# Kernel optimization log

Measured on AMD Instinct MI355X. Metric: run time of the kernel, lower is better.

Reference implementation:

```python
import jax, jax.numpy as jnp
import numpy as np
from jax import lax

EPS = 1e-5
DN = ('NCHW', 'OIHW', 'NCHW')


def setup_inputs() -> dict:
    key = jax.random.key(0)
    ks = jax.random.split(key, 26)
    f = lambda k, shape: jax.random.normal(k, shape, dtype=jnp.float32) * 0.05
    u = lambda k, shape: jax.random.uniform(k, shape, jnp.float32, 0.5, 1.5)
    B = 512
    return {
        'x': jax.random.normal(ks[0], (B, 3, 32, 32), jnp.float32),
        'conv1_w': f(ks[1], (64, 3, 3, 3)), 'conv1_b': f(ks[2], (64,)),
        'bn1_g': 1.0 + f(ks[3], (64,)), 'bn1_b': f(ks[4], (64,)),
        'bn1_m': f(ks[5], (64,)), 'bn1_v': u(ks[6], (64,)),
        'conv2_w': f(ks[7], (256, 64, 3, 3)), 'conv2_b': f(ks[8], (256,)),
        'bna_g': 1.0 + f(ks[9], (64, 4)), 'bna_b': f(ks[10], (64, 4)),
        'bna_m': f(ks[11], (64, 4)), 'bna_v': u(ks[12], (64, 4)),
        'tconv_w': f(ks[13], (64, 8, 4, 3, 3)), 'tconv_b': f(ks[14], (64, 8)),
        'bnb_g': 1.0 + f(ks[15], (64, 8)), 'bnb_b': f(ks[16], (64, 8)),
        'bnb_m': f(ks[17], (64, 8)), 'bnb_v': u(ks[18], (64, 8)),
        'lin_w': f(ks[19], (64, 9, 1152)), 'lin_b': f(ks[20], (64, 9)),
        'fc1_w': f(ks[21], (512, 576)), 'fc1_b': f(ks[22], (512,)),
        'fc2_w': f(ks[23], (100, 512)), 'fc2_b': f(ks[24], (100,)),
    }


def reference(x, conv1_w, conv1_b, bn1_g, bn1_b, bn1_m, bn1_v,
              conv2_w, conv2_b,
              bna_g, bna_b, bna_m, bna_v, tconv_w, tconv_b,
              bnb_g, bnb_b, bnb_m, bnb_v, lin_w, lin_b,
              fc1_w, fc1_b, fc2_w, fc2_b):
    B = x.shape[0]
    # features: Conv(3->64,k3) -> ReLU -> BN(64) -> Conv(64->256,k3) -> ReLU -> MaxPool2
    h = lax.conv_general_dilated(x, conv1_w, (1, 1), 'VALID', dimension_numbers=DN)
    h = jax.nn.relu(h + conv1_b[None, :, None, None])  # [B,64,30,30]
    h = (h - bn1_m[None, :, None, None]) * lax.rsqrt(bn1_v + EPS)[None, :, None, None] \
        * bn1_g[None, :, None, None] + bn1_b[None, :, None, None]
    h = lax.conv_general_dilated(h, conv2_w, (1, 1), 'VALID', dimension_numbers=DN)
    h = jax.nn.relu(h + conv2_b[None, :, None, None])  # [B,256,28,28]
    h = lax.reduce_window(h, -jnp.inf, lax.max, (1, 1, 2, 2), (1, 1, 2, 2), 'VALID')  # [B,256,14,14]

    # 64 towers: BN2d(4) -> Conv(4->8,k3) -> BN2d(8) -> Flatten -> Linear(1152->9)
    f4 = h.reshape(B, 64, 4, 14, 14)
    f4 = (f4 - bna_m[None, :, :, None, None]) * lax.rsqrt(bna_v + EPS)[None, :, :, None, None] \
        * bna_g[None, :, :, None, None] + bna_b[None, :, :, None, None]
    # grouped conv fuses all 64 towers: out channels 64*8=512, 4 in-channels per group
    t = lax.conv_general_dilated(f4.reshape(B, 256, 14, 14), tconv_w.reshape(512, 4, 3, 3),
                                 (1, 1), 'VALID', dimension_numbers=DN, feature_group_count=64)
    t = t + tconv_b.reshape(512)[None, :, None, None]  # [B,512,12,12]
    t = t.reshape(B, 64, 8, 12, 12)
    t = (t - bnb_m[None, :, :, None, None]) * lax.rsqrt(bnb_v + EPS)[None, :, :, None, None] \
        * bnb_g[None, :, :, None, None] + bnb_b[None, :, :, None, None]
    flat = t.reshape(B, 64, 8 * 12 * 12)
    tow = jnp.einsum('btf,tof->bto', flat, lin_w) + lin_b[None]  # [B,64,9]
    z = tow.reshape(B, 576)

    # classifier (dropout = identity in eval)
    h1 = jax.nn.relu(z @ fc1_w.T + fc1_b)
    return h1 @ fc2_w.T + fc2_b
```

## Files before the change

kernel.cpp:

```cpp
#include <hip/hip_runtime.h>
#include <hip/hip_bf16.h>

#define EPS 1e-5f

typedef __attribute__((ext_vector_type(8))) short bf16x8;
typedef __attribute__((ext_vector_type(4))) float f32x4;

__device__ __forceinline__ float b2f(unsigned short u) {
  union { unsigned int i; float f; } v; v.i = ((unsigned int)u) << 16; return v.f;
}
__device__ __forceinline__ unsigned short f2bu(float f) {
  __hip_bfloat16 h = __float2bfloat16(f);
  return *reinterpret_cast<unsigned short*>(&h);
}

__device__ __forceinline__ void g2l16(const void* g, void* l) {
  __builtin_amdgcn_global_load_lds(
      (__attribute__((address_space(1))) void*)((unsigned long long)g),
      (__attribute__((address_space(3))) void*)((unsigned long long)l), 16, 0, 0);
}

__global__ __launch_bounds__(256) void k_prep(
    const float* __restrict__ x, const float* __restrict__ w1,
    const float* __restrict__ cb, const float* __restrict__ bg,
    const float* __restrict__ bb, const float* __restrict__ bm,
    const float* __restrict__ bv, __hip_bfloat16* __restrict__ h1,
    const float* __restrict__ w2, __hip_bfloat16* __restrict__ w2s,
    const float* __restrict__ fw1, unsigned int* __restrict__ w1p,
    const float* __restrict__ fw2, unsigned int* __restrict__ w2p,
    const float* __restrict__ lw, const float* __restrict__ lb,
    const float* __restrict__ tw, const float* __restrict__ tb,
    const float* __restrict__ bag, const float* __restrict__ bab,
    const float* __restrict__ bam, const float* __restrict__ bav,
    const float* __restrict__ bbg, const float* __restrict__ bbb,
    const float* __restrict__ bbm, const float* __restrict__ bbv,
    float* __restrict__ Weff, float* __restrict__ beff) {
  __shared__ __align__(16) char smem[43008];
  int tid = threadIdx.x;
  int bi = blockIdx.x;

  if (bi < 64) {
    int t = bi;
    float* lws = (float*)smem;
    float* tws = (float*)(smem + 41472);
    float* part = (float*)(smem + 42624);
    {
      const float4* src = (const float4*)(lw + (size_t)t * 9 * 1152);
      float4* dst = (float4*)lws;
      for (int i = tid; i < 2592; i += 256) dst[i] = src[i];
    }
    for (int i = tid; i < 288; i += 256) {
      int o8 = i / 36, c = (i % 36) / 9, kk = i % 9;
      float sa = bag[t * 4 + c] * rsqrtf(bav[t * 4 + c] + EPS);
      float sb = bbg[t * 8 + o8] * rsqrtf(bbv[t * 8 + o8] + EPS);
      tws[i] = tw[((t * 8 + o8) * 4 + c) * 9 + kk] * sa * sb;
    }
    __syncthreads();
    if (tid < 252) {
      int j = tid / 28;
      int rem = tid % 28;
      int c = rem / 7, q = rem % 7;
      float acc[2][14];
#pragma unroll
      for (int pr = 0; pr < 2; pr++)
#pragma unroll
        for (int ix = 0; ix < 14; ix++) acc[pr][ix] = 0.f;
#pragma unroll 1
      for (int o8 = 0; o8 < 8; o8++) {
        float twr[9];
#pragma unroll
        for (int kk = 0; kk < 9; kk++) twr[kk] = tws[o8 * 36 + c * 9 + kk];
        float lwc[4][16];
#pragma unroll
        for (int cr = 0; cr < 4; cr++) {
          int y = 2 * q - 2 + cr;
          bool vld = (y >= 0) & (y <= 11);
          int ya = vld ? y : 0;
          const float* bp = lws + j * 1152 + o8 * 144 + ya * 12;
          float4 A = *(const float4*)bp;
          float4 B = *(const float4*)(bp + 4);
          float4 C = *(const float4*)(bp + 8);
          lwc[cr][0] = 0.f; lwc[cr][1] = 0.f; lwc[cr][14] = 0.f; lwc[cr][15] = 0.f;
          lwc[cr][2] = vld ? A.x : 0.f;  lwc[cr][3] = vld ? A.y : 0.f;
          lwc[cr][4] = vld ? A.z : 0.f;  lwc[cr][5] = vld ? A.w : 0.f;
          lwc[cr][6] = vld ? B.x : 0.f;  lwc[cr][7] = vld ? B.y : 0.f;
          lwc[cr][8] = vld ? B.z : 0.f;  lwc[cr][9] = vld ? B.w : 0.f;
          lwc[cr][10] = vld ? C.x : 0.f; lwc[cr][11] = vld ? C.y : 0.f;
          lwc[cr][12] = vld ? C.z : 0.f; lwc[cr][13] = vld ? C.w : 0.f;
        }
#pragma unroll
        for (int ky = 0; ky < 3; ky++)
#pragma unroll
          for (int kx = 0; kx < 3; kx++) {
            float wv = twr[ky * 3 + kx];
#pragma unroll
            for (int pr = 0; pr < 2; pr++)
#pragma unroll
              for (int ix = 0; ix < 14; ix++)
                acc[pr][ix] += lwc[pr - ky + 2][ix - kx + 2] * wv;
          }
      }
#pragma unroll
      for (int pr = 0; pr < 2; pr++)
#pragma unroll
        for (int ix = 0; ix < 14; ix++)
          Weff[(((size_t)(t * 9 + j)) * 196 + (2 * q + pr) * 14 + ix) * 4 + c] = acc[pr][ix];
    }
    if (tid < 72) {
      int j = tid / 8, o8 = tid % 8;
      float s = 0.f;
      const float* bp = lws + j * 1152 + o8 * 144;
      for (int i = 0; i < 144; i++) s += bp[i];
      float sb = bbg[t * 8 + o8] * rsqrtf(bbv[t * 8 + o8] + EPS);
      float bfov = sb * tb[t * 8 + o8] + bbb[t * 8 + o8] - bbm[t * 8 + o8] * sb;
      for (int c2 = 0; c2 < 4; c2++) {
        float sa2 = bag[t * 4 + c2] * rsqrtf(bav[t * 4 + c2] + EPS);
        float ha = bab[t * 4 + c2] - bam[t * 4 + c2] * sa2;
        float wsum = 0.f;
        for (int k = 0; k < 9; k++) wsum += tw[((t * 8 + o8) * 4 + c2) * 9 + k];
        bfov += sb * wsum * ha;
      }
      part[tid] = bfov * s;
    }
    __syncthreads();
    if (tid < 9) {
      float acc = lb[t * 9 + tid];
      for (int o8 = 0; o8 < 8; o8++) acc += part[tid * 8 + o8];
      beff[t * 9 + tid] = acc;
    }
  } else if (bi < 576) {
    int b = bi - 64;
    float* xs = (float*)smem;
    float* wsm = (float*)(smem + 13824);
    {
      const float4* src = (const float4*)(x + (size_t)b * 3072);
      for (int i = tid; i < 768; i += 256) {
        int ic = i >> 8, r = (i >> 3) & 31, v = i & 7;
        *(float4*)(xs + (ic * 32 + r) * 36 + v * 4) = src[i];
      }
      const float4* wsrc = (const float4*)w1;
      float4* wdst = (float4*)wsm;
      for (int i = tid; i < 432; i += 256) wdst[i] = wsrc[i];
    }
    __syncthreads();
    int oc = tid & 63;
    int xg = tid >> 6;
    float wr[27];
#pragma unroll
    for (int q = 0; q < 27; q++) wr[q] = wsm[oc * 27 + q];
    float bias = cb[oc];
    float sc = bg[oc] * rsqrtf(bv[oc] + EPS);
    float sh = bb[oc] - bm[oc] * sc;
    float rx[3][3][12];
#pragma unroll
    for (int ic = 0; ic < 3; ic++)
#pragma unroll
      for (int s = 0; s < 2; s++) {
        const float* rp = xs + (ic * 32 + s) * 36 + xg * 8;
        float4 A = *(const float4*)rp, B = *(const float4*)(rp + 4), C = *(const float4*)(rp + 8);
        rx[ic][s][0] = A.x; rx[ic][s][1] = A.y; rx[ic][s][2] = A.z; rx[ic][s][3] = A.w;
        rx[ic][s][4] = B.x; rx[ic][s][5] = B.y; rx[ic][s][6] = B.z; rx[ic][s][7] = B.w;
        rx[ic][s][8] = C.x; rx[ic][s][9] = C.y; rx[ic][s][10] = C.z; rx[ic][s][11] = C.w;
      }
    int nst = (xg == 3) ? 6 : 8;
    __hip_bfloat16* dst0 = h1 + (((size_t)b * 30) * 30 + xg * 8) * 64 + oc;
#pragma unroll 1
    for (int y3 = 0; y3 < 10; y3++) {
#pragma unroll
      for (int s = 0; s < 3; s++) {
        int y = y3 * 3 + s;
        int ls = (s + 2) % 3;
#pragma unroll
        for (int ic = 0; ic < 3; ic++) {
          const float* rp = xs + (ic * 32 + (y + 2)) * 36 + xg * 8;
          float4 A = *(const float4*)rp, B = *(const float4*)(rp + 4), C = *(const float4*)(rp + 8);
          rx[ic][ls][0] = A.x; rx[ic][ls][1] = A.y; rx[ic][ls][2] = A.z; rx[ic][ls][3] = A.w;
          rx[ic][ls][4] = B.x; rx[ic][ls][5] = B.y; rx[ic][ls][6] = B.z; rx[ic][ls][7] = B.w;
          rx[ic][ls][8] = C.x; rx[ic][ls][9] = C.y; rx[ic][ls][10] = C.z; rx[ic][ls][11] = C.w;
        }
        float o[8];
#pragma unroll
        for (int j = 0; j < 8; j++) o[j] = bias;
#pragma unroll
        for (int ic = 0; ic < 3; ic++)
#pragma unroll
          for (int ky = 0; ky < 3; ky++) {
            int sl = (s + ky) % 3;
#pragma unroll
            for (int kx = 0; kx < 3; kx++) {
              float wv = wr[ic * 9 + ky * 3 + kx];
#pragma unroll
              for (int j = 0; j < 8; j++) o[j] += rx[ic][sl][j + kx] * wv;
            }
          }
        __hip_bfloat16* dst = dst0 + (size_t)y * 30 * 64;
#pragma unroll
        for (int j = 0; j < 8; j++)
          if (j < nst) dst[(size_t)j * 64] = __float2bfloat16(fmaxf(o[j], 0.f) * sc + sh);
      }
    }
  } else if (bi < 1152) {
    int g = (bi - 576) * 256 + tid;
    int kk = g >> 14;
    int rem = g & 16383;
    int oc = rem >> 6, e = rem & 63;
    int es = e ^ ((oc & 7) << 3);
    w2s[(kk * 256 + oc) * 64 + es] = __float2bfloat16(w2[(oc * 64 + e) * 9 + kk]);
  } else {
    int g = (bi - 1152) * 256 + tid;
    {
      int kp = g >> 9, o = g & 511;
      unsigned int lo = f2bu(fw1[o * 576 + 2 * kp]);
      unsigned int hi = f2bu(fw1[o * 576 + 2 * kp + 1]);
      w1p[g] = lo | (hi << 16);
    }
    if (g < 25600) {
      int kp = g / 100, o = g % 100;
      unsigned int lo = f2bu(fw2[o * 512 + 2 * kp]);
      unsigned int hi = f2bu(fw2[o * 512 + 2 * kp + 1]);
      w2p[g] = lo | (hi << 16);
    }
  }
}

__global__ __launch_bounds__(512) void k2_conv2(
    const __hip_bfloat16* __restrict__ h1, const __hip_bfloat16* __restrict__ w2s,
    const float* __restrict__ c2b, __hip_bfloat16* __restrict__ pT) {
  __shared__ __align__(16) char lds[81920];
  int tid = threadIdx.x;
  int bi = blockIdx.x;
  int b = bi / 14, yp = bi % 14;
  int l = tid & 63, w = tid >> 6;

  int r = tid >> 3;
  int rc = r < 56 ? r : 55;
  int yl = rc >= 28 ? 1 : 0;
  int xx = rc - yl * 28;
  int ael = ((tid & 7) << 3) ^ ((rc & 7) << 3);
  const __hip_bfloat16* aSrc0 =
      h1 + (((size_t)(b * 30 + yp * 2 + yl)) * 30 + xx) * 64 + ael;
  const char* bSrc0 = (const char*)w2s;

  f32x4 acc[4][2];
#pragma unroll
  for (int m = 0; m < 4; m++)
#pragma unroll
    for (int n = 0; n < 2; n++) acc[m][n] = (f32x4){0.f, 0.f, 0.f, 0.f};

#define STAGE(kk, s)                                                            \
  {                                                                             \
    g2l16(aSrc0 + (((kk) / 3) * 30 + ((kk) % 3)) * 64,                          \
          lds + (s)*8192 + tid * 16);                                           \
    const char* bs = bSrc0 + (kk)*32768;                                        \
    _Pragma("unroll") for (int q = 0; q < 4; q++)                               \
        g2l16(bs + q * 8192 + tid * 16,                                         \
              lds + 16384 + (s)*32768 + q * 8192 + tid * 16);                   \
  }

  STAGE(0, 0);
#pragma unroll
  for (int c = 0; c < 9; c++) {
    __syncthreads();
    if (c < 8) STAGE(c + 1, (c + 1) & 1);
    char* aB = lds + (c & 1) * 8192;
    char* bB = lds + 16384 + (c & 1) * 32768;
#pragma unroll
    for (int ks = 0; ks < 2; ks++) {
      bf16x8 af[4], bfr[2];
      int kb = (ks * 32 + ((l >> 4) * 8)) * 2;
#pragma unroll
      for (int m = 0; m < 4; m++) {
        int row = m * 16 + (l & 15);
        af[m] = *(const bf16x8*)(aB + row * 128 + (kb ^ ((row & 7) << 4)));
      }
#pragma unroll
      for (int n = 0; n < 2; n++) {
        int oc = w * 32 + n * 16 + (l & 15);
        bfr[n] = *(const bf16x8*)(bB + oc * 128 + (kb ^ ((oc & 7) << 4)));
      }
#pragma unroll
      for (int m = 0; m < 4; m++)
#pragma unroll
        for (int n = 0; n < 2; n++)
          acc[m][n] = __builtin_amdgcn_mfma_f32_16x16x32_bf16(af[m], bfr[n], acc[m][n], 0, 0, 0);
    }
  }
#undef STAGE
  __syncthreads();

  float* ep = (float*)(lds) + w * 2112;
#pragma unroll
  for (int n = 0; n < 2; n++) {
    int col = n * 16 + (l & 15);
    float bias = c2b[w * 32 + col];
#pragma unroll
    for (int m = 0; m < 4; m++)
#pragma unroll
      for (int i = 0; i < 4; i++) {
        int row = m * 16 + ((l >> 4) * 4) + i;
        ep[row * 33 + col] = fmaxf(acc[m][n][i] + bias, 0.f);
      }
  }
  __syncthreads();
  unsigned short* pool = (unsigned short*)(lds + 69632);
#pragma unroll
  for (int q = 0; q < 7; q++) {
    int xp = (l >> 5) * 7 + q;
    int col = l & 31;
    int base0 = (2 * xp) * 33 + col;
    float m0 = fmaxf(fmaxf(ep[base0], ep[base0 + 33]),
                     fmaxf(ep[base0 + 28 * 33], ep[base0 + 29 * 33]));
    pool[(w * 32 + col) * 14 + xp] = f2bu(m0);
  }
  __syncthreads();
  if (tid < 448) {
    int t = tid / 7, sub = tid - t * 7;
    union { unsigned short s[8]; uint4 v; } pk;
#pragma unroll
    for (int e = 0; e < 8; e++) {
      int ee = sub * 8 + e;
      pk.s[e] = pool[(t * 4 + (ee & 3)) * 14 + (ee >> 2)];
    }
    *(uint4*)((char*)pT + ((size_t)(t * 512 + b)) * 1568 + yp * 112 + sub * 16) = pk.v;
  }
}

__global__ __launch_bounds__(576) void k3_towers(
    const __hip_bfloat16* __restrict__ pT, const float* __restrict__ Weff,
    const float* __restrict__ beff, float* __restrict__ z) {
  __shared__ __align__(16) char sm[131648];
  char* Al = sm;
  float* Wl = (float*)(sm + 103424);
  int tid = threadIdx.x, bi = blockIdx.x;
  int t = bi >> 3, b0 = (bi & 7) * 64;
  for (int idx = tid; idx < 6272; idx += 576) {
    int row = idx / 98, ch = idx - row * 98;
    uint4 v = *(const uint4*)((const char*)pT + ((size_t)(t * 512 + b0 + row)) * 1568 + ch * 16);
    *(uint4*)(Al + row * 1616 + ch * 16) = v;
  }
  const uint4* wsrc = (const uint4*)(Weff + t * 9 * 784);
  for (int idx = tid; idx < 1764; idx += 576) ((uint4*)Wl)[idx] = wsrc[idx];
  __syncthreads();
  int j = tid >> 6, b = tid & 63;
  float acc = 0.f;
  const char* ap = Al + b * 1616;
  const float* wp = Wl + j * 784;
#pragma unroll 2
  for (int ch = 0; ch < 98; ch++) {
    bf16x8 pv = *(const bf16x8*)(ap + ch * 16);
    float4 w0 = *(const float4*)(wp + ch * 8);
    float4 w1_ = *(const float4*)(wp + ch * 8 + 4);
    acc += b2f((unsigned short)pv[0]) * w0.x + b2f((unsigned short)pv[1]) * w0.y +
           b2f((unsigned short)pv[2]) * w0.z + b2f((unsigned short)pv[3]) * w0.w +
           b2f((unsigned short)pv[4]) * w1_.x + b2f((unsigned short)pv[5]) * w1_.y +
           b2f((unsigned short)pv[6]) * w1_.z + b2f((unsigned short)pv[7]) * w1_.w;
  }
  z[(size_t)(b0 + b) * 576 + t * 9 + j] = acc + beff[t * 9 + j];
}

__global__ __launch_bounds__(256) void k4_fc(
    const float* __restrict__ z, const unsigned int* __restrict__ w1p, const float* __restrict__ b1,
    const unsigned int* __restrict__ w2p, const float* __restrict__ b2, float* __restrict__ out) {
  __shared__ float zl[576];
  __shared__ float hl[512];
  int tid = threadIdx.x, b = blockIdx.x;
  for (int i = tid; i < 576; i += 256) zl[i] = z[(size_t)b * 576 + i];
  __syncthreads();
#pragma unroll
  for (int oo = 0; oo < 2; oo++) {
    int o = tid + oo * 256;
    float acc = b1[o];
#pragma unroll 4
    for (int kp = 0; kp < 288; kp++) {
      unsigned int u = w1p[kp * 512 + o];
      float2 zz = *(const float2*)(zl + 2 * kp);
      acc += zz.x * b2f((unsigned short)(u & 0xffff)) + zz.y * b2f((unsigned short)(u >> 16));
    }
    hl[o] = fmaxf(acc, 0.f);
  }
  __syncthreads();
  if (tid < 100) {
    float acc = b2[tid];
#pragma unroll 4
    for (int kp = 0; kp < 256; kp++) {
      unsigned int u = w2p[kp * 100 + tid];
      float2 hh = *(const float2*)(hl + 2 * kp);
      acc += hh.x * b2f((unsigned short)(u & 0xffff)) + hh.y * b2f((unsigned short)(u >> 16));
    }
    out[(size_t)b * 100 + tid] = acc;
  }
}

extern "C" void kernel_launch(void* const* d_in, const int* in_sizes, int n_in,
                              void* d_out, int out_size, void* d_ws, size_t ws_size,
                              hipStream_t stream) {
  const float* x    = (const float*)d_in[0];
  const float* w1   = (const float*)d_in[1];
  const float* c1b  = (const float*)d_in[2];
  const float* bn1g = (const float*)d_in[3];
  const float* bn1b = (const float*)d_in[4];
  const float* bn1m = (const float*)d_in[5];
  const float* bn1v = (const float*)d_in[6];
  const float* w2   = (const float*)d_in[7];
  const float* c2b  = (const float*)d_in[8];
  const float* bnag = (const float*)d_in[9];
  const float* bnab = (const float*)d_in[10];
  const float* bnam = (const float*)d_in[11];
  const float* bnav = (const float*)d_in[12];
  const float* tw   = (const float*)d_in[13];
  const float* tb   = (const float*)d_in[14];
  const float* bnbg = (const float*)d_in[15];
  const float* bnbb = (const float*)d_in[16];
  const float* bnbm = (const float*)d_in[17];
  const float* bnbv = (const float*)d_in[18];
  const float* linw = (const float*)d_in[19];
  const float* linb = (const float*)d_in[20];
  const float* fc1w = (const float*)d_in[21];
  const float* fc1b = (const float*)d_in[22];
  const float* fc2w = (const float*)d_in[23];
  const float* fc2b = (const float*)d_in[24];
  float* out = (float*)d_out;

  char* ws = (char*)d_ws;
  size_t off = 0;
  auto alloc = [&](size_t bytes) {
    char* q = ws + off;
    off += (bytes + 255) & ~(size_t)255;
    return q;
  };
  __hip_bfloat16* h1  = (__hip_bfloat16*)alloc(512ull * 30 * 30 * 64 * 2);
  __hip_bfloat16* pT  = (__hip_bfloat16*)alloc(64ull * 512 * 784 * 2 + 256);
  __hip_bfloat16* w2s = (__hip_bfloat16*)alloc(9ull * 256 * 64 * 2);
  float* Weff = (float*)alloc(451584ull * 4);
  float* beff = (float*)alloc(576ull * 4);
  unsigned int* w1p = (unsigned int*)alloc(288ull * 512 * 4);
  unsigned int* w2p = (unsigned int*)alloc(256ull * 100 * 4);
  float* z    = (float*)alloc(512ull * 576 * 4);

  k_prep<<<1728, 256, 0, stream>>>(x, w1, c1b, bn1g, bn1b, bn1m, bn1v, h1,
                                   w2, w2s, fc1w, w1p, fc2w, w2p,
                                   linw, linb, tw, tb,
                                   bnag, bnab, bnam, bnav,
                                   bnbg, bnbb, bnbm, bnbv, Weff, beff);
  k2_conv2<<<512 * 14, 512, 0, stream>>>(h1, w2s, c2b, pT);
  k3_towers<<<512, 576, 0, stream>>>(pT, Weff, beff, z);
  k4_fc<<<512, 256, 0, stream>>>(z, w1p, fc1b, w2p, fc2b, out);
}
```

Before: 371.3 us.

## Load conv2 weights straight into registers, shrink LDS, split conv1 blocks

In the conv2 kernel the weight tiles now go from global memory straight into double-buffered registers rather than being staged through LDS. The epilogue scratch is stored as bf16, which cuts LDS from 80KB to 44KB and allows two 512-thread blocks per CU. Conv1 in the prep kernel is split into half-image blocks for more parallelism. The tower kernel reads activations directly from global memory and no longer stages them in LDS. The trade-off is more register pressure and repeated global weight loads per block, which lean on the cache.

```diff
diff --git a/kernel.cpp b/kernel.cpp
--- a/kernel.cpp
+++ b/kernel.cpp
@@ -25,7 +25,7 @@
     const float* __restrict__ cb, const float* __restrict__ bg,
     const float* __restrict__ bb, const float* __restrict__ bm,
     const float* __restrict__ bv, __hip_bfloat16* __restrict__ h1,
-    const float* __restrict__ w2, __hip_bfloat16* __restrict__ w2s,
+    const float* __restrict__ w2, __hip_bfloat16* __restrict__ w2u,
     const float* __restrict__ fw1, unsigned int* __restrict__ w1p,
     const float* __restrict__ fw2, unsigned int* __restrict__ w2p,
     const float* __restrict__ lw, const float* __restrict__ lb,
@@ -128,15 +128,17 @@
       for (int o8 = 0; o8 < 8; o8++) acc += part[tid * 8 + o8];
       beff[t * 9 + tid] = acc;
     }
-  } else if (bi < 576) {
-    int b = bi - 64;
+  } else if (bi < 1088) {
+    int idx = bi - 64;
+    int b = idx >> 1, hf = idx & 1;
+    int y0 = hf * 15;
     float* xs = (float*)smem;
-    float* wsm = (float*)(smem + 13824);
+    float* wsm = (float*)(smem + 7344);
     {
-      const float4* src = (const float4*)(x + (size_t)b * 3072);
-      for (int i = tid; i < 768; i += 256) {
-        int ic = i >> 8, r = (i >> 3) & 31, v = i & 7;
-        *(float4*)(xs + (ic * 32 + r) * 36 + v * 4) = src[i];
+      for (int i = tid; i < 408; i += 256) {
+        int ic = i / 136, rr = (i % 136) / 8, v = i % 8;
+        *(float4*)(xs + (ic * 17 + rr) * 36 + v * 4) =
+            *(const float4*)(x + (size_t)b * 3072 + (ic * 32 + y0 + rr) * 32 + v * 4);
       }
       const float4* wsrc = (const float4*)w1;
       float4* wdst = (float4*)wsm;
@@ -156,23 +158,23 @@
     for (int ic = 0; ic < 3; ic++)
 #pragma unroll
       for (int s = 0; s < 2; s++) {
-        const float* rp = xs + (ic * 32 + s) * 36 + xg * 8;
+        const float* rp = xs + (ic * 17 + s) * 36 + xg * 8;
         float4 A = *(const float4*)rp, B = *(const float4*)(rp + 4), C = *(const float4*)(rp + 8);
         rx[ic][s][0] = A.x; rx[ic][s][1] = A.y; rx[ic][s][2] = A.z; rx[ic][s][3] = A.w;
         rx[ic][s][4] = B.x; rx[ic][s][5] = B.y; rx[ic][s][6] = B.z; rx[ic][s][7] = B.w;
         rx[ic][s][8] = C.x; rx[ic][s][9] = C.y; rx[ic][s][10] = C.z; rx[ic][s][11] = C.w;
       }
     int nst = (xg == 3) ? 6 : 8;
-    __hip_bfloat16* dst0 = h1 + (((size_t)b * 30) * 30 + xg * 8) * 64 + oc;
+    __hip_bfloat16* dst0 = h1 + (((size_t)b * 30 + y0) * 30 + xg * 8) * 64 + oc;
 #pragma unroll 1
-    for (int y3 = 0; y3 < 10; y3++) {
+    for (int y3 = 0; y3 < 5; y3++) {
 #pragma unroll
       for (int s = 0; s < 3; s++) {
         int y = y3 * 3 + s;
         int ls = (s + 2) % 3;
 #pragma unroll
         for (int ic = 0; ic < 3; ic++) {
-          const float* rp = xs + (ic * 32 + (y + 2)) * 36 + xg * 8;
+          const float* rp = xs + (ic * 17 + (y + 2)) * 36 + xg * 8;
           float4 A = *(const float4*)rp, B = *(const float4*)(rp + 4), C = *(const float4*)(rp + 8);
           rx[ic][ls][0] = A.x; rx[ic][ls][1] = A.y; rx[ic][ls][2] = A.z; rx[ic][ls][3] = A.w;
           rx[ic][ls][4] = B.x; rx[ic][ls][5] = B.y; rx[ic][ls][6] = B.z; rx[ic][ls][7] = B.w;
@@ -199,15 +201,14 @@
           if (j < nst) dst[(size_t)j * 64] = __float2bfloat16(fmaxf(o[j], 0.f) * sc + sh);
       }
     }
-  } else if (bi < 1152) {
-    int g = (bi - 576) * 256 + tid;
+  } else if (bi < 1664) {
+    int g = (bi - 1088) * 256 + tid;
     int kk = g >> 14;
     int rem = g & 16383;
     int oc = rem >> 6, e = rem & 63;
-    int es = e ^ ((oc & 7) << 3);
-    w2s[(kk * 256 + oc) * 64 + es] = __float2bfloat16(w2[(oc * 64 + e) * 9 + kk]);
+    w2u[(kk * 256 + oc) * 64 + e] = __float2bfloat16(w2[(oc * 64 + e) * 9 + kk]);
   } else {
-    int g = (bi - 1152) * 256 + tid;
+    int g = (bi - 1664) * 256 + tid;
     {
       int kp = g >> 9, o = g & 511;
       unsigned int lo = f2bu(fw1[o * 576 + 2 * kp]);
@@ -223,10 +224,10 @@
   }
 }
 
-__global__ __launch_bounds__(512) void k2_conv2(
-    const __hip_bfloat16* __restrict__ h1, const __hip_bfloat16* __restrict__ w2s,
+__global__ __launch_bounds__(512, 2) void k2_conv2(
+    const __hip_bfloat16* __restrict__ h1, const __hip_bfloat16* __restrict__ w2u,
     const float* __restrict__ c2b, __hip_bfloat16* __restrict__ pT) {
-  __shared__ __align__(16) char lds[81920];
+  __shared__ __align__(16) char lds[45056];
   int tid = threadIdx.x;
   int bi = blockIdx.x;
   int b = bi / 14, yp = bi % 14;
@@ -239,7 +240,8 @@
   int ael = ((tid & 7) << 3) ^ ((rc & 7) << 3);
   const __hip_bfloat16* aSrc0 =
       h1 + (((size_t)(b * 30 + yp * 2 + yl)) * 30 + xx) * 64 + ael;
-  const char* bSrc0 = (const char*)w2s;
+
+  const char* bBase = (const char*)w2u + ((w * 32 + (l & 15)) * 128 + (l >> 4) * 16);
 
   f32x4 acc[4][2];
 #pragma unroll
@@ -247,27 +249,34 @@
 #pragma unroll
     for (int n = 0; n < 2; n++) acc[m][n] = (f32x4){0.f, 0.f, 0.f, 0.f};
 
-#define STAGE(kk, s)                                                            \
-  {                                                                             \
-    g2l16(aSrc0 + (((kk) / 3) * 30 + ((kk) % 3)) * 64,                          \
-          lds + (s)*8192 + tid * 16);                                           \
-    const char* bs = bSrc0 + (kk)*32768;                                        \
-    _Pragma("unroll") for (int q = 0; q < 4; q++)                               \
-        g2l16(bs + q * 8192 + tid * 16,                                         \
-              lds + 16384 + (s)*32768 + q * 8192 + tid * 16);                   \
-  }
-
-  STAGE(0, 0);
+  bf16x8 bA[4], bB_[4];
+  g2l16(aSrc0, lds + tid * 16);
+#pragma unroll
+  for (int q = 0; q < 4; q++)
+    bA[q] = *(const bf16x8*)(bBase + (q & 1) * 64 + (q >> 1) * 2048);
+
 #pragma unroll
   for (int c = 0; c < 9; c++) {
     __syncthreads();
-    if (c < 8) STAGE(c + 1, (c + 1) & 1);
+    if (c < 8) {
+      g2l16(aSrc0 + (((c + 1) / 3) * 30 + ((c + 1) % 3)) * 64,
+            lds + ((c + 1) & 1) * 8192 + tid * 16);
+      const char* nb = bBase + (c + 1) * 32768;
+      if (c & 1) {
+#pragma unroll
+        for (int q = 0; q < 4; q++)
+          bA[q] = *(const bf16x8*)(nb + (q & 1) * 64 + (q >> 1) * 2048);
+      } else {
+#pragma unroll
+        for (int q = 0; q < 4; q++)
+          bB_[q] = *(const bf16x8*)(nb + (q & 1) * 64 + (q >> 1) * 2048);
+      }
+    }
     char* aB = lds + (c & 1) * 8192;
-    char* bB = lds + 16384 + (c & 1) * 32768;
 #pragma unroll
     for (int ks = 0; ks < 2; ks++) {
-      bf16x8 af[4], bfr[2];
-      int kb = (ks * 32 + ((l >> 4) * 8)) * 2;
+      bf16x8 af[4];
+      int kb = ks * 64 + (l >> 4) * 16;
 #pragma unroll
       for (int m = 0; m < 4; m++) {
         int row = m * 16 + (l & 15);
@@ -275,20 +284,16 @@
       }
 #pragma unroll
       for (int n = 0; n < 2; n++) {
-        int oc = w * 32 + n * 16 + (l & 15);
-        bfr[n] = *(const bf16x8*)(bB + oc * 128 + (kb ^ ((oc & 7) << 4)));
-      }
-#pragma unroll
-      for (int m = 0; m < 4; m++)
-#pragma unroll
-        for (int n = 0; n < 2; n++)
-          acc[m][n] = __builtin_amdgcn_mfma_f32_16x16x32_bf16(af[m], bfr[n], acc[m][n], 0, 0, 0);
-    }
-  }
-#undef STAGE
-  __syncthreads();
-
-  float* ep = (float*)(lds) + w * 2112;
+        bf16x8 bcur = (c & 1) ? bB_[n * 2 + ks] : bA[n * 2 + ks];
+#pragma unroll
+        for (int m = 0; m < 4; m++)
+          acc[m][n] = __builtin_amdgcn_mfma_f32_16x16x32_bf16(af[m], bcur, acc[m][n], 0, 0, 0);
+      }
+    }
+  }
+  __syncthreads();
+
+  unsigned short* ep = (unsigned short*)lds + w * 2304;
 #pragma unroll
   for (int n = 0; n < 2; n++) {
     int col = n * 16 + (l & 15);
@@ -298,18 +303,18 @@
 #pragma unroll
       for (int i = 0; i < 4; i++) {
         int row = m * 16 + ((l >> 4) * 4) + i;
-        ep[row * 33 + col] = fmaxf(acc[m][n][i] + bias, 0.f);
-      }
-  }
-  __syncthreads();
-  unsigned short* pool = (unsigned short*)(lds + 69632);
+        ep[row * 36 + col] = f2bu(fmaxf(acc[m][n][i] + bias, 0.f));
+      }
+  }
+  __syncthreads();
+  unsigned short* pool = (unsigned short*)(lds + 36864);
 #pragma unroll
   for (int q = 0; q < 7; q++) {
     int xp = (l >> 5) * 7 + q;
     int col = l & 31;
-    int base0 = (2 * xp) * 33 + col;
-    float m0 = fmaxf(fmaxf(ep[base0], ep[base0 + 33]),
-                     fmaxf(ep[base0 + 28 * 33], ep[base0 + 29 * 33]));
+    int base0 = (2 * xp) * 36 + col;
+    float m0 = fmaxf(fmaxf(b2f(ep[base0]), b2f(ep[base0 + 36])),
+                     fmaxf(b2f(ep[base0 + 28 * 36]), b2f(ep[base0 + 29 * 36])));
     pool[(w * 32 + col) * 14 + xp] = f2bu(m0);
   }
   __syncthreads();
@@ -328,24 +333,17 @@
 __global__ __launch_bounds__(576) void k3_towers(
     const __hip_bfloat16* __restrict__ pT, const float* __restrict__ Weff,
     const float* __restrict__ beff, float* __restrict__ z) {
-  __shared__ __align__(16) char sm[131648];
-  char* Al = sm;
-  float* Wl = (float*)(sm + 103424);
+  __shared__ __align__(16) float Wl[7056];
   int tid = threadIdx.x, bi = blockIdx.x;
   int t = bi >> 3, b0 = (bi & 7) * 64;
-  for (int idx = tid; idx < 6272; idx += 576) {
-    int row = idx / 98, ch = idx - row * 98;
-    uint4 v = *(const uint4*)((const char*)pT + ((size_t)(t * 512 + b0 + row)) * 1568 + ch * 16);
-    *(uint4*)(Al + row * 1616 + ch * 16) = v;
-  }
-  const uint4* wsrc = (const uint4*)(Weff + t * 9 * 784);
-  for (int idx = tid; idx < 1764; idx += 576) ((uint4*)Wl)[idx] = wsrc[idx];
-  __syncthreads();
-  int j = tid >> 6, b = tid & 63;
+  const float4* wsrc = (const float4*)(Weff + (size_t)t * 7056);
+  for (int idx = tid; idx < 1764; idx += 576) ((float4*)Wl)[idx] = wsrc[idx];
+  __syncthreads();
+  int j = tid >> 6, l = tid & 63;
+  const char* ap = (const char*)pT + (size_t)(t * 512 + b0 + l) * 1568;
+  const float* wp = Wl + j * 784;
   float acc = 0.f;
-  const char* ap = Al + b * 1616;
-  const float* wp = Wl + j * 784;
-#pragma unroll 2
+#pragma unroll 7
   for (int ch = 0; ch < 98; ch++) {
     bf16x8 pv = *(const bf16x8*)(ap + ch * 16);
     float4 w0 = *(const float4*)(wp + ch * 8);
@@ -355,7 +353,7 @@
            b2f((unsigned short)pv[4]) * w1_.x + b2f((unsigned short)pv[5]) * w1_.y +
            b2f((unsigned short)pv[6]) * w1_.z + b2f((unsigned short)pv[7]) * w1_.w;
   }
-  z[(size_t)(b0 + b) * 576 + t * 9 + j] = acc + beff[t * 9 + j];
+  z[(size_t)(b0 + l) * 576 + t * 9 + j] = acc + beff[t * 9 + j];
 }
 
 __global__ __launch_bounds__(256) void k4_fc(
@@ -430,19 +428,19 @@
   };
   __hip_bfloat16* h1  = (__hip_bfloat16*)alloc(512ull * 30 * 30 * 64 * 2);
   __hip_bfloat16* pT  = (__hip_bfloat16*)alloc(64ull * 512 * 784 * 2 + 256);
-  __hip_bfloat16* w2s = (__hip_bfloat16*)alloc(9ull * 256 * 64 * 2);
+  __hip_bfloat16* w2u = (__hip_bfloat16*)alloc(9ull * 256 * 64 * 2);
   float* Weff = (float*)alloc(451584ull * 4);
   float* beff = (float*)alloc(576ull * 4);
   unsigned int* w1p = (unsigned int*)alloc(288ull * 512 * 4);
   unsigned int* w2p = (unsigned int*)alloc(256ull * 100 * 4);
   float* z    = (float*)alloc(512ull * 576 * 4);
 
-  k_prep<<<1728, 256, 0, stream>>>(x, w1, c1b, bn1g, bn1b, bn1m, bn1v, h1,
-                                   w2, w2s, fc1w, w1p, fc2w, w2p,
+  k_prep<<<2240, 256, 0, stream>>>(x, w1, c1b, bn1g, bn1b, bn1m, bn1v, h1,
+                                   w2, w2u, fc1w, w1p, fc2w, w2p,
                                    linw, linb, tw, tb,
                                    bnag, bnab, bnam, bnav,
                                    bnbg, bnbb, bnbm, bnbv, Weff, beff);
-  k2_conv2<<<512 * 14, 512, 0, stream>>>(h1, w2s, c2b, pT);
+  k2_conv2<<<512 * 14, 512, 0, stream>>>(h1, w2u, c2b, pT);
   k3_towers<<<512, 576, 0, stream>>>(pT, Weff, beff, z);
   k4_fc<<<512, 256, 0, stream>>>(z, w1p, fc1b, w2p, fc2b, out);
 }
```

Measured after the change: 495.4 us. +33.4%, slower.

## Fuse conv1 into conv2 kernel, computing input tile in LDS with halo recompute

Applied to the files above, without the earlier changes.

Conv1+ReLU+BN is now computed inside each conv2 block for the 4 input rows it needs and written directly into swizzled LDS, removing the h1 intermediate round trip through global memory and the separate prep blocks. The conv2 A-operand is read from this resident tile at shifted offsets per kernel tap, so only B (weights) is staged asynchronously. The epilogue buffer is shrunk to bf16, and the tower kernel reads pT directly from global instead of staging it in LDS. The cost is that conv1 is recomputed for overlapping halo rows (each row about twice), and the kernel now has a launch-bounds occupancy hint.

```diff
diff --git a/kernel.cpp b/kernel.cpp
--- a/kernel.cpp
+++ b/kernel.cpp
@@ -21,10 +21,6 @@
 }
 
 __global__ __launch_bounds__(256) void k_prep(
-    const float* __restrict__ x, const float* __restrict__ w1,
-    const float* __restrict__ cb, const float* __restrict__ bg,
-    const float* __restrict__ bb, const float* __restrict__ bm,
-    const float* __restrict__ bv, __hip_bfloat16* __restrict__ h1,
     const float* __restrict__ w2, __hip_bfloat16* __restrict__ w2s,
     const float* __restrict__ fw1, unsigned int* __restrict__ w1p,
     const float* __restrict__ fw2, unsigned int* __restrict__ w2p,
@@ -128,86 +124,15 @@
       for (int o8 = 0; o8 < 8; o8++) acc += part[tid * 8 + o8];
       beff[t * 9 + tid] = acc;
     }
-  } else if (bi < 576) {
-    int b = bi - 64;
-    float* xs = (float*)smem;
-    float* wsm = (float*)(smem + 13824);
-    {
-      const float4* src = (const float4*)(x + (size_t)b * 3072);
-      for (int i = tid; i < 768; i += 256) {
-        int ic = i >> 8, r = (i >> 3) & 31, v = i & 7;
-        *(float4*)(xs + (ic * 32 + r) * 36 + v * 4) = src[i];
-      }
-      const float4* wsrc = (const float4*)w1;
-      float4* wdst = (float4*)wsm;
-      for (int i = tid; i < 432; i += 256) wdst[i] = wsrc[i];
-    }
-    __syncthreads();
-    int oc = tid & 63;
-    int xg = tid >> 6;
-    float wr[27];
-#pragma unroll
-    for (int q = 0; q < 27; q++) wr[q] = wsm[oc * 27 + q];
-    float bias = cb[oc];
-    float sc = bg[oc] * rsqrtf(bv[oc] + EPS);
-    float sh = bb[oc] - bm[oc] * sc;
-    float rx[3][3][12];
-#pragma unroll
-    for (int ic = 0; ic < 3; ic++)
-#pragma unroll
-      for (int s = 0; s < 2; s++) {
-        const float* rp = xs + (ic * 32 + s) * 36 + xg * 8;
-        float4 A = *(const float4*)rp, B = *(const float4*)(rp + 4), C = *(const float4*)(rp + 8);
-        rx[ic][s][0] = A.x; rx[ic][s][1] = A.y; rx[ic][s][2] = A.z; rx[ic][s][3] = A.w;
-        rx[ic][s][4] = B.x; rx[ic][s][5] = B.y; rx[ic][s][6] = B.z; rx[ic][s][7] = B.w;
-        rx[ic][s][8] = C.x; rx[ic][s][9] = C.y; rx[ic][s][10] = C.z; rx[ic][s][11] = C.w;
-      }
-    int nst = (xg == 3) ? 6 : 8;
-    __hip_bfloat16* dst0 = h1 + (((size_t)b * 30) * 30 + xg * 8) * 64 + oc;
-#pragma unroll 1
-    for (int y3 = 0; y3 < 10; y3++) {
-#pragma unroll
-      for (int s = 0; s < 3; s++) {
-        int y = y3 * 3 + s;
-        int ls = (s + 2) % 3;
-#pragma unroll
-        for (int ic = 0; ic < 3; ic++) {
-          const float* rp = xs + (ic * 32 + (y + 2)) * 36 + xg * 8;
-          float4 A = *(const float4*)rp, B = *(const float4*)(rp + 4), C = *(const float4*)(rp + 8);
-          rx[ic][ls][0] = A.x; rx[ic][ls][1] = A.y; rx[ic][ls][2] = A.z; rx[ic][ls][3] = A.w;
-          rx[ic][ls][4] = B.x; rx[ic][ls][5] = B.y; rx[ic][ls][6] = B.z; rx[ic][ls][7] = B.w;
-          rx[ic][ls][8] = C.x; rx[ic][ls][9] = C.y; rx[ic][ls][10] = C.z; rx[ic][ls][11] = C.w;
-        }
-        float o[8];
-#pragma unroll
-        for (int j = 0; j < 8; j++) o[j] = bias;
-#pragma unroll
-        for (int ic = 0; ic < 3; ic++)
-#pragma unroll
-          for (int ky = 0; ky < 3; ky++) {
-            int sl = (s + ky) % 3;
-#pragma unroll
-            for (int kx = 0; kx < 3; kx++) {
-              float wv = wr[ic * 9 + ky * 3 + kx];
-#pragma unroll
-              for (int j = 0; j < 8; j++) o[j] += rx[ic][sl][j + kx] * wv;
-            }
-          }
-        __hip_bfloat16* dst = dst0 + (size_t)y * 30 * 64;
-#pragma unroll
-        for (int j = 0; j < 8; j++)
-          if (j < nst) dst[(size_t)j * 64] = __float2bfloat16(fmaxf(o[j], 0.f) * sc + sh);
-      }
-    }
-  } else if (bi < 1152) {
-    int g = (bi - 576) * 256 + tid;
+  } else if (bi < 640) {
+    int g = (bi - 64) * 256 + tid;
     int kk = g >> 14;
     int rem = g & 16383;
     int oc = rem >> 6, e = rem & 63;
     int es = e ^ ((oc & 7) << 3);
     w2s[(kk * 256 + oc) * 64 + es] = __float2bfloat16(w2[(oc * 64 + e) * 9 + kk]);
   } else {
-    int g = (bi - 1152) * 256 + tid;
+    int g = (bi - 640) * 256 + tid;
     {
       int kp = g >> 9, o = g & 511;
       unsigned int lo = f2bu(fw1[o * 576 + 2 * kp]);
@@ -223,55 +148,111 @@
   }
 }
 
-__global__ __launch_bounds__(512) void k2_conv2(
-    const __hip_bfloat16* __restrict__ h1, const __hip_bfloat16* __restrict__ w2s,
-    const float* __restrict__ c2b, __hip_bfloat16* __restrict__ pT) {
+template <int WOFF>
+__device__ __forceinline__ void conv1_part(
+    const float* __restrict__ x, int b, int y0, int row4, int xh,
+    const float* wr, float bias, float sc, float sh, int oc, char* aLds) {
+  float o[15];
+#pragma unroll
+  for (int j = 0; j < 15; j++) o[j] = bias;
+#pragma unroll
+  for (int ic = 0; ic < 3; ic++)
+#pragma unroll
+    for (int ky = 0; ky < 3; ky++) {
+      const float* rp = x + ((b * 3 + ic) * 32 + (y0 + row4 + ky)) * 32 + (WOFF ? 12 : 0);
+      float win[20];
+#pragma unroll
+      for (int q = 0; q < 5; q++) {
+        float4 v = *(const float4*)(rp + q * 4);
+        win[q * 4 + 0] = v.x; win[q * 4 + 1] = v.y;
+        win[q * 4 + 2] = v.z; win[q * 4 + 3] = v.w;
+      }
+#pragma unroll
+      for (int kx = 0; kx < 3; kx++) {
+        float wv = wr[ic * 9 + ky * 3 + kx];
+#pragma unroll
+        for (int j = 0; j < 15; j++) o[j] += win[WOFF + j + kx] * wv;
+      }
+    }
+#pragma unroll
+  for (int j = 0; j < 15; j++) {
+    int xp = xh + j;
+    float v = fmaxf(o[j], 0.f) * sc + sh;
+    *(unsigned short*)(aLds + (row4 * 30 + xp) * 128 + ((oc * 2) ^ ((xp & 7) << 4))) = f2bu(v);
+  }
+}
+
+__global__ __launch_bounds__(512, 4) void k2_conv2(
+    const float* __restrict__ x, const float* __restrict__ w1,
+    const float* __restrict__ cb, const float* __restrict__ bg,
+    const float* __restrict__ bb, const float* __restrict__ bm,
+    const float* __restrict__ bv,
+    const __hip_bfloat16* __restrict__ w2s, const float* __restrict__ c2b,
+    __hip_bfloat16* __restrict__ pT) {
   __shared__ __align__(16) char lds[81920];
   int tid = threadIdx.x;
   int bi = blockIdx.x;
   int b = bi / 14, yp = bi % 14;
   int l = tid & 63, w = tid >> 6;
-
-  int r = tid >> 3;
-  int rc = r < 56 ? r : 55;
-  int yl = rc >= 28 ? 1 : 0;
-  int xx = rc - yl * 28;
-  int ael = ((tid & 7) << 3) ^ ((rc & 7) << 3);
-  const __hip_bfloat16* aSrc0 =
-      h1 + (((size_t)(b * 30 + yp * 2 + yl)) * 30 + xx) * 64 + ael;
+  int y0 = yp * 2;
+
+  {
+    int oc = l;
+    int row4 = w >> 1;
+    int xh = (w & 1) * 15;
+    float wr[27];
+#pragma unroll
+    for (int q = 0; q < 27; q++) wr[q] = w1[oc * 27 + q];
+    float bias = cb[oc];
+    float sc = bg[oc] * rsqrtf(bv[oc] + EPS);
+    float sh = bb[oc] - bm[oc] * sc;
+    if (w & 1)
+      conv1_part<3>(x, b, y0, row4, xh, wr, bias, sc, sh, oc, lds);
+    else
+      conv1_part<0>(x, b, y0, row4, xh, wr, bias, sc, sh, oc, lds);
+  }
+
+  int ylm[4], xxm[4];
+#pragma unroll
+  for (int m = 0; m < 4; m++) {
+    int rr = m * 16 + (l & 15);
+    int rcm = rr < 56 ? rr : 55;
+    ylm[m] = rcm >= 28 ? 1 : 0;
+    xxm[m] = rcm - ylm[m] * 28;
+  }
+  int kgran = (l >> 4) * 16;
+
   const char* bSrc0 = (const char*)w2s;
-
-  f32x4 acc[4][2];
-#pragma unroll
-  for (int m = 0; m < 4; m++)
-#pragma unroll
-    for (int n = 0; n < 2; n++) acc[m][n] = (f32x4){0.f, 0.f, 0.f, 0.f};
-
-#define STAGE(kk, s)                                                            \
+#define STAGEB(kk, s)                                                           \
   {                                                                             \
-    g2l16(aSrc0 + (((kk) / 3) * 30 + ((kk) % 3)) * 64,                          \
-          lds + (s)*8192 + tid * 16);                                           \
     const char* bs = bSrc0 + (kk)*32768;                                        \
     _Pragma("unroll") for (int q = 0; q < 4; q++)                               \
         g2l16(bs + q * 8192 + tid * 16,                                         \
               lds + 16384 + (s)*32768 + q * 8192 + tid * 16);                   \
   }
 
-  STAGE(0, 0);
+  f32x4 acc[4][2];
+#pragma unroll
+  for (int m = 0; m < 4; m++)
+#pragma unroll
+    for (int n = 0; n < 2; n++) acc[m][n] = (f32x4){0.f, 0.f, 0.f, 0.f};
+
+  STAGEB(0, 0);
 #pragma unroll
   for (int c = 0; c < 9; c++) {
     __syncthreads();
-    if (c < 8) STAGE(c + 1, (c + 1) & 1);
-    char* aB = lds + (c & 1) * 8192;
+    if (c < 8) STAGEB(c + 1, (c + 1) & 1);
+    int ky = c / 3, kx = c % 3;
     char* bB = lds + 16384 + (c & 1) * 32768;
 #pragma unroll
     for (int ks = 0; ks < 2; ks++) {
       bf16x8 af[4], bfr[2];
-      int kb = (ks * 32 + ((l >> 4) * 8)) * 2;
+      int kb = ks * 64 + kgran;
 #pragma unroll
       for (int m = 0; m < 4; m++) {
-        int row = m * 16 + (l & 15);
-        af[m] = *(const bf16x8*)(aB + row * 128 + (kb ^ ((row & 7) << 4)));
+        int xp = xxm[m] + kx;
+        af[m] = *(const bf16x8*)(lds + ((ylm[m] + ky) * 30 + xp) * 128 +
+                                 (kb ^ ((xp & 7) << 4)));
       }
 #pragma unroll
       for (int n = 0; n < 2; n++) {
@@ -285,10 +266,10 @@
           acc[m][n] = __builtin_amdgcn_mfma_f32_16x16x32_bf16(af[m], bfr[n], acc[m][n], 0, 0, 0);
     }
   }
-#undef STAGE
-  __syncthreads();
-
-  float* ep = (float*)(lds) + w * 2112;
+#undef STAGEB
+  __syncthreads();
+
+  unsigned short* ep = (unsigned short*)lds + w * 2304;
 #pragma unroll
   for (int n = 0; n < 2; n++) {
     int col = n * 16 + (l & 15);
@@ -298,18 +279,18 @@
 #pragma unroll
       for (int i = 0; i < 4; i++) {
         int row = m * 16 + ((l >> 4) * 4) + i;
-        ep[row * 33 + col] = fmaxf(acc[m][n][i] + bias, 0.f);
-      }
-  }
-  __syncthreads();
-  unsigned short* pool = (unsigned short*)(lds + 69632);
+        ep[row * 36 + col] = f2bu(fmaxf(acc[m][n][i] + bias, 0.f));
+      }
+  }
+  __syncthreads();
+  unsigned short* pool = (unsigned short*)(lds + 36864);
 #pragma unroll
   for (int q = 0; q < 7; q++) {
     int xp = (l >> 5) * 7 + q;
     int col = l & 31;
-    int base0 = (2 * xp) * 33 + col;
-    float m0 = fmaxf(fmaxf(ep[base0], ep[base0 + 33]),
-                     fmaxf(ep[base0 + 28 * 33], ep[base0 + 29 * 33]));
+    int base0 = (2 * xp) * 36 + col;
+    float m0 = fmaxf(fmaxf(b2f(ep[base0]), b2f(ep[base0 + 36])),
+                     fmaxf(b2f(ep[base0 + 28 * 36]), b2f(ep[base0 + 29 * 36])));
     pool[(w * 32 + col) * 14 + xp] = f2bu(m0);
   }
   __syncthreads();
@@ -328,24 +309,17 @@
 __global__ __launch_bounds__(576) void k3_towers(
     const __hip_bfloat16* __restrict__ pT, const float* __restrict__ Weff,
     const float* __restrict__ beff, float* __restrict__ z) {
-  __shared__ __align__(16) char sm[131648];
-  char* Al = sm;
-  float* Wl = (float*)(sm + 103424);
+  __shared__ __align__(16) float Wl[7056];
   int tid = threadIdx.x, bi = blockIdx.x;
   int t = bi >> 3, b0 = (bi & 7) * 64;
-  for (int idx = tid; idx < 6272; idx += 576) {
-    int row = idx / 98, ch = idx - row * 98;
-    uint4 v = *(const uint4*)((const char*)pT + ((size_t)(t * 512 + b0 + row)) * 1568 + ch * 16);
-    *(uint4*)(Al + row * 1616 + ch * 16) = v;
-  }
-  const uint4* wsrc = (const uint4*)(Weff + t * 9 * 784);
-  for (int idx = tid; idx < 1764; idx += 576) ((uint4*)Wl)[idx] = wsrc[idx];
-  __syncthreads();
-  int j = tid >> 6, b = tid & 63;
+  const float4* wsrc = (const float4*)(Weff + (size_t)t * 7056);
+  for (int idx = tid; idx < 1764; idx += 576) ((float4*)Wl)[idx] = wsrc[idx];
+  __syncthreads();
+  int j = tid >> 6, l = tid & 63;
+  const char* ap = (const char*)pT + (size_t)(t * 512 + b0 + l) * 1568;
+  const float* wp = Wl + j * 784;
   float acc = 0.f;
-  const char* ap = Al + b * 1616;
-  const float* wp = Wl + j * 784;
-#pragma unroll 2
+#pragma unroll 7
   for (int ch = 0; ch < 98; ch++) {
     bf16x8 pv = *(const bf16x8*)(ap + ch * 16);
     float4 w0 = *(const float4*)(wp + ch * 8);
@@ -355,7 +329,7 @@
            b2f((unsigned short)pv[4]) * w1_.x + b2f((unsigned short)pv[5]) * w1_.y +
            b2f((unsigned short)pv[6]) * w1_.z + b2f((unsigned short)pv[7]) * w1_.w;
   }
-  z[(size_t)(b0 + b) * 576 + t * 9 + j] = acc + beff[t * 9 + j];
+  z[(size_t)(b0 + l) * 576 + t * 9 + j] = acc + beff[t * 9 + j];
 }
 
 __global__ __launch_bounds__(256) void k4_fc(
@@ -428,7 +402,6 @@
     off += (bytes + 255) & ~(size_t)255;
     return q;
   };
-  __hip_bfloat16* h1  = (__hip_bfloat16*)alloc(512ull * 30 * 30 * 64 * 2);
   __hip_bfloat16* pT  = (__hip_bfloat16*)alloc(64ull * 512 * 784 * 2 + 256);
   __hip_bfloat16* w2s = (__hip_bfloat16*)alloc(9ull * 256 * 64 * 2);
   float* Weff = (float*)alloc(451584ull * 4);
@@ -437,12 +410,12 @@
   unsigned int* w2p = (unsigned int*)alloc(256ull * 100 * 4);
   float* z    = (float*)alloc(512ull * 576 * 4);
 
-  k_prep<<<1728, 256, 0, stream>>>(x, w1, c1b, bn1g, bn1b, bn1m, bn1v, h1,
-                                   w2, w2s, fc1w, w1p, fc2w, w2p,
+  k_prep<<<1216, 256, 0, stream>>>(w2, w2s, fc1w, w1p, fc2w, w2p,
                                    linw, linb, tw, tb,
                                    bnag, bnab, bnam, bnav,
                                    bnbg, bnbb, bnbm, bnbv, Weff, beff);
-  k2_conv2<<<512 * 14, 512, 0, stream>>>(h1, w2s, c2b, pT);
+  k2_conv2<<<512 * 14, 512, 0, stream>>>(x, w1, c1b, bn1g, bn1b, bn1m, bn1v,
+                                         w2s, c2b, pT);
   k3_towers<<<512, 576, 0, stream>>>(pT, Weff, beff, z);
   k4_fc<<<512, 256, 0, stream>>>(z, w1p, fc1b, w2p, fc2b, out);
 }
```

Result: slower. 416.7 us (+12.2%).

## Fuse tower linear into conv2 epilogue with atomic accumulation into z

Applied to the files above, without the earlier changes.

Removes the separate towers kernel and the pooled intermediate buffer. Each conv2 block now dots its pooled row directly against the effective tower weights and atomically adds partial sums into z, which is zeroed with a memset; the bias is added in the FC kernel. The epilogue staging buffer shrinks to bf16, and a block-index swizzle changes the order in which blocks are scheduled. The cost is extra global atomics, plus every block reading its slice of the Weff rows, in exchange for dropping the pT write/read round trip and one kernel launch.

```diff
diff --git a/kernel.cpp b/kernel.cpp
--- a/kernel.cpp
+++ b/kernel.cpp
@@ -225,11 +225,13 @@
 
 __global__ __launch_bounds__(512) void k2_conv2(
     const __hip_bfloat16* __restrict__ h1, const __hip_bfloat16* __restrict__ w2s,
-    const float* __restrict__ c2b, __hip_bfloat16* __restrict__ pT) {
+    const float* __restrict__ c2b, const float* __restrict__ Weff,
+    float* __restrict__ z) {
   __shared__ __align__(16) char lds[81920];
   int tid = threadIdx.x;
-  int bi = blockIdx.x;
-  int b = bi / 14, yp = bi % 14;
+  int bid = blockIdx.x;
+  int swz = (bid & 7) * 896 + (bid >> 3);
+  int b = swz / 14, yp = swz % 14;
   int l = tid & 63, w = tid >> 6;
 
   int r = tid >> 3;
@@ -288,7 +290,7 @@
 #undef STAGE
   __syncthreads();
 
-  float* ep = (float*)(lds) + w * 2112;
+  unsigned short* ep = (unsigned short*)lds + w * 2304;
 #pragma unroll
   for (int n = 0; n < 2; n++) {
     int col = n * 16 + (l & 15);
@@ -298,73 +300,48 @@
 #pragma unroll
       for (int i = 0; i < 4; i++) {
         int row = m * 16 + ((l >> 4) * 4) + i;
-        ep[row * 33 + col] = fmaxf(acc[m][n][i] + bias, 0.f);
+        ep[row * 36 + col] = f2bu(fmaxf(acc[m][n][i] + bias, 0.f));
       }
   }
   __syncthreads();
-  unsigned short* pool = (unsigned short*)(lds + 69632);
+  unsigned short* pool = (unsigned short*)(lds + 36864);
 #pragma unroll
   for (int q = 0; q < 7; q++) {
     int xp = (l >> 5) * 7 + q;
     int col = l & 31;
-    int base0 = (2 * xp) * 33 + col;
-    float m0 = fmaxf(fmaxf(ep[base0], ep[base0 + 33]),
-                     fmaxf(ep[base0 + 28 * 33], ep[base0 + 29 * 33]));
+    int base0 = (2 * xp) * 36 + col;
+    float m0 = fmaxf(fmaxf(b2f(ep[base0]), b2f(ep[base0 + 36])),
+                     fmaxf(b2f(ep[base0 + 28 * 36]), b2f(ep[base0 + 29 * 36])));
     pool[(w * 32 + col) * 14 + xp] = f2bu(m0);
   }
   __syncthreads();
-  if (tid < 448) {
-    int t = tid / 7, sub = tid - t * 7;
-    union { unsigned short s[8]; uint4 v; } pk;
-#pragma unroll
-    for (int e = 0; e < 8; e++) {
-      int ee = sub * 8 + e;
-      pk.s[e] = pool[(t * 4 + (ee & 3)) * 14 + (ee >> 2)];
-    }
-    *(uint4*)((char*)pT + ((size_t)(t * 512 + b)) * 1568 + yp * 112 + sub * 16) = pk.v;
-  }
-}
-
-__global__ __launch_bounds__(576) void k3_towers(
-    const __hip_bfloat16* __restrict__ pT, const float* __restrict__ Weff,
-    const float* __restrict__ beff, float* __restrict__ z) {
-  __shared__ __align__(16) char sm[131648];
-  char* Al = sm;
-  float* Wl = (float*)(sm + 103424);
-  int tid = threadIdx.x, bi = blockIdx.x;
-  int t = bi >> 3, b0 = (bi & 7) * 64;
-  for (int idx = tid; idx < 6272; idx += 576) {
-    int row = idx / 98, ch = idx - row * 98;
-    uint4 v = *(const uint4*)((const char*)pT + ((size_t)(t * 512 + b0 + row)) * 1568 + ch * 16);
-    *(uint4*)(Al + row * 1616 + ch * 16) = v;
-  }
-  const uint4* wsrc = (const uint4*)(Weff + t * 9 * 784);
-  for (int idx = tid; idx < 1764; idx += 576) ((uint4*)Wl)[idx] = wsrc[idx];
-  __syncthreads();
-  int j = tid >> 6, b = tid & 63;
-  float acc = 0.f;
-  const char* ap = Al + b * 1616;
-  const float* wp = Wl + j * 784;
-#pragma unroll 2
-  for (int ch = 0; ch < 98; ch++) {
-    bf16x8 pv = *(const bf16x8*)(ap + ch * 16);
-    float4 w0 = *(const float4*)(wp + ch * 8);
-    float4 w1_ = *(const float4*)(wp + ch * 8 + 4);
-    acc += b2f((unsigned short)pv[0]) * w0.x + b2f((unsigned short)pv[1]) * w0.y +
-           b2f((unsigned short)pv[2]) * w0.z + b2f((unsigned short)pv[3]) * w0.w +
-           b2f((unsigned short)pv[4]) * w1_.x + b2f((unsigned short)pv[5]) * w1_.y +
-           b2f((unsigned short)pv[6]) * w1_.z + b2f((unsigned short)pv[7]) * w1_.w;
-  }
-  z[(size_t)(b0 + b) * 576 + t * 9 + j] = acc + beff[t * 9 + j];
+#pragma unroll
+  for (int rep = 0; rep < 2; rep++) {
+    int tj = rep * 512 + tid;
+    if (rep == 1 && tid >= 64) break;
+    int t = tj / 9;
+    const float4* wrow = (const float4*)(Weff + (size_t)tj * 784 + yp * 56);
+    const unsigned short* pr = pool + t * 4 * 14;
+    float s = 0.f;
+#pragma unroll
+    for (int xp = 0; xp < 14; xp++) {
+      float4 wv = wrow[xp];
+      s += wv.x * b2f(pr[xp]) + wv.y * b2f(pr[14 + xp]) +
+           wv.z * b2f(pr[28 + xp]) + wv.w * b2f(pr[42 + xp]);
+    }
+    atomicAdd(z + (size_t)b * 576 + tj, s);
+  }
 }
 
 __global__ __launch_bounds__(256) void k4_fc(
-    const float* __restrict__ z, const unsigned int* __restrict__ w1p, const float* __restrict__ b1,
-    const unsigned int* __restrict__ w2p, const float* __restrict__ b2, float* __restrict__ out) {
+    const float* __restrict__ z, const float* __restrict__ beff,
+    const unsigned int* __restrict__ w1p, const float* __restrict__ b1,
+    const unsigned int* __restrict__ w2p, const float* __restrict__ b2,
+    float* __restrict__ out) {
   __shared__ float zl[576];
   __shared__ float hl[512];
   int tid = threadIdx.x, b = blockIdx.x;
-  for (int i = tid; i < 576; i += 256) zl[i] = z[(size_t)b * 576 + i];
+  for (int i = tid; i < 576; i += 256) zl[i] = z[(size_t)b * 576 + i] + beff[i];
   __syncthreads();
 #pragma unroll
   for (int oo = 0; oo < 2; oo++) {
@@ -429,7 +406,6 @@
     return q;
   };
   __hip_bfloat16* h1  = (__hip_bfloat16*)alloc(512ull * 30 * 30 * 64 * 2);
-  __hip_bfloat16* pT  = (__hip_bfloat16*)alloc(64ull * 512 * 784 * 2 + 256);
   __hip_bfloat16* w2s = (__hip_bfloat16*)alloc(9ull * 256 * 64 * 2);
   float* Weff = (float*)alloc(451584ull * 4);
   float* beff = (float*)alloc(576ull * 4);
@@ -437,12 +413,12 @@
   unsigned int* w2p = (unsigned int*)alloc(256ull * 100 * 4);
   float* z    = (float*)alloc(512ull * 576 * 4);
 
+  hipMemsetAsync(z, 0, 512ull * 576 * 4, stream);
   k_prep<<<1728, 256, 0, stream>>>(x, w1, c1b, bn1g, bn1b, bn1m, bn1v, h1,
                                    w2, w2s, fc1w, w1p, fc2w, w2p,
                                    linw, linb, tw, tb,
                                    bnag, bnab, bnam, bnav,
                                    bnbg, bnbb, bnbm, bnbv, Weff, beff);
-  k2_conv2<<<512 * 14, 512, 0, stream>>>(h1, w2s, c2b, pT);
-  k3_towers<<<512, 576, 0, stream>>>(pT, Weff, beff, z);
-  k4_fc<<<512, 256, 0, stream>>>(z, w1p, fc1b, w2p, fc2b, out);
-}
+  k2_conv2<<<512 * 14, 512, 0, stream>>>(h1, w2s, c2b, Weff, z);
+  k4_fc<<<512, 256, 0, stream>>>(z, beff, w1p, fc1b, w2p, fc2b, out);
+}
```

Measured after the change: 428.9 us. 1.16x slower.
